# Performance work log

Hardware: AMD Instinct MI355X
Metric: run time of the kernel (lower is better)

The kernel has to match this reference:

```python
import jax, jax.numpy as jnp
import numpy as np
import math

D_MODEL = 1024
NUM_HEADS = 16
D_K = 64
B, T = 2, 2048


def setup_inputs() -> dict:
    key = jax.random.key(0)
    ks = jax.random.split(key, 12)
    s = 0.02
    return {
        "Q": jax.random.normal(ks[0], (B, T, D_MODEL), jnp.float32),
        "K": jax.random.normal(ks[1], (B, T, D_MODEL), jnp.float32),
        "V": jax.random.normal(ks[2], (B, T, D_MODEL), jnp.float32),
        # stacked per-head projection weights: [H, d_model, d_k]
        "Wq": jax.random.normal(ks[3], (NUM_HEADS, D_MODEL, D_K), jnp.float32) * s,
        "bq": jax.random.normal(ks[4], (NUM_HEADS, D_K), jnp.float32) * s,
        "Wk": jax.random.normal(ks[5], (NUM_HEADS, D_MODEL, D_K), jnp.float32) * s,
        "bk": jax.random.normal(ks[6], (NUM_HEADS, D_K), jnp.float32) * s,
        "Wv": jax.random.normal(ks[7], (NUM_HEADS, D_MODEL, D_K), jnp.float32) * s,
        "bv": jax.random.normal(ks[8], (NUM_HEADS, D_K), jnp.float32) * s,
        "Wo": jax.random.normal(ks[9], (D_MODEL, D_MODEL), jnp.float32) * s,
        "bo": jax.random.normal(ks[10], (D_MODEL,), jnp.float32) * s,
    }


def reference(Q, K, V, Wq, bq, Wk, bk, Wv, bv, Wo, bo):
    scale = 1.0 / math.sqrt(D_K)
    # fused batched per-head projections (replaces the Python per-head loop)
    Qh = jnp.einsum("btd,hdk->bhtk", Q, Wq) + bq[None, :, None, :]
    Kh = jnp.einsum("btd,hdk->bhtk", K, Wk) + bk[None, :, None, :]
    Vh = jnp.einsum("btd,hdk->bhtk", V, Wv) + bv[None, :, None, :]
    scores = jnp.einsum("bhtk,bhsk->bhts", Qh, Kh) * scale  # [B,H,T,T]
    attn = jax.nn.softmax(scores, axis=-1)
    ctx = jnp.einsum("bhts,bhsk->bhtk", attn, Vh)  # [B,H,T,d_k]
    # Faithful to the original: plain view of contiguous [B,H,T,d] into
    # [B,T,H*d] WITHOUT transposing head/time (matches torch .view semantics).
    bsz, nt = Q.shape[0], Q.shape[1]
    x = ctx.reshape(bsz, nt, NUM_HEADS * D_K)
    out = x @ Wo.T + bo
    # dropout with p=0.0 is identity; omitted for determinism
    return out
```

## Files before the change

kernel.cpp:

```cpp
#include <hip/hip_runtime.h>
#include <stdint.h>

typedef __attribute__((ext_vector_type(8))) short short8;
typedef __attribute__((ext_vector_type(4))) short short4v;
typedef __attribute__((ext_vector_type(4))) float float4v;

#define MFMA16(a, b, c) __builtin_amdgcn_mfma_f32_16x16x32_bf16((a), (b), (c), 0, 0, 0)

__device__ __forceinline__ ushort f2bf_rne(float f) {
  union { float f; unsigned u; } x; x.f = f;
  unsigned r = x.u + 0x7FFFu + ((x.u >> 16) & 1u);
  return (ushort)(r >> 16);
}
__device__ __forceinline__ ushort f2bf_trunc(float f) {
  union { float f; unsigned u; } x; x.f = f;
  return (ushort)(x.u >> 16);
}
__device__ __forceinline__ void gload16(const ushort* g, ushort* lds) {
  __builtin_amdgcn_global_load_lds(
      (__attribute__((address_space(1))) unsigned int*)g,
      (__attribute__((address_space(3))) unsigned int*)lds, 16, 0, 0);
}

__global__ __launch_bounds__(256) void cvt4_kernel(
    const float* __restrict__ s0, const float* __restrict__ s1,
    const float* __restrict__ s2, const float* __restrict__ s3,
    ushort* __restrict__ d0, ushort* __restrict__ d1, ushort* __restrict__ d2,
    ushort* __restrict__ d3) {
  const int plane = blockIdx.y;
  const int n = (plane == 3) ? (1 << 20) : (1 << 22);
  const int i = (blockIdx.x * 256 + threadIdx.x) * 8;
  if (i >= n) return;
  const float* s = plane == 0 ? s0 : (plane == 1 ? s1 : (plane == 2 ? s2 : s3));
  ushort* d = plane == 0 ? d0 : (plane == 1 ? d1 : (plane == 2 ? d2 : d3));
  float4 a = *(const float4*)(s + i);
  float4 b = *(const float4*)(s + i + 4);
  ushort t[8] __attribute__((aligned(16))) = {
      f2bf_rne(a.x), f2bf_rne(a.y), f2bf_rne(a.z), f2bf_rne(a.w),
      f2bf_rne(b.x), f2bf_rne(b.y), f2bf_rne(b.z), f2bf_rne(b.w)};
  *(uint4*)(d + i) = *(const uint4*)t;
}

__device__ __forceinline__ void transpose64f(const float* __restrict__ in, int is,
                                             ushort* __restrict__ out, int os,
                                             ushort* lds ) {
  const int t = threadIdx.x;
#pragma unroll
  for (int it = 0; it < 2; ++it) {
    int e = it * 2048 + t * 8;
    int r = e >> 6, c = e & 63;
    const float* p = in + (size_t)r * is + c;
    float4 x0 = *(const float4*)p;
    float4 x1 = *(const float4*)(p + 4);
    ushort tv[8] __attribute__((aligned(16))) = {
        f2bf_rne(x0.x), f2bf_rne(x0.y), f2bf_rne(x0.z), f2bf_rne(x0.w),
        f2bf_rne(x1.x), f2bf_rne(x1.y), f2bf_rne(x1.z), f2bf_rne(x1.w)};
    *(uint4*)&lds[r * 72 + c] = *(const uint4*)tv;
  }
  __syncthreads();
  const int cc = t >> 2;
  const int rg = (t & 3) * 16;
  ushort tmp[16] __attribute__((aligned(16)));
#pragma unroll
  for (int i = 0; i < 16; ++i) tmp[i] = lds[(rg + i) * 72 + cc];
  *(uint4*)&out[(size_t)cc * os + rg] = *(const uint4*)&tmp[0];
  *(uint4*)&out[(size_t)cc * os + rg + 8] = *(const uint4*)&tmp[8];
}

__global__ __launch_bounds__(256, 2) void repack_w_kernel(
    const float* __restrict__ Wq, const float* __restrict__ Wk,
    const float* __restrict__ Wv, ushort* __restrict__ BtQ, ushort* __restrict__ BtK,
    ushort* __restrict__ BtV) {
  __shared__ ushort lds[64 * 72];
  const float* W = blockIdx.z == 0 ? Wq : (blockIdx.z == 1 ? Wk : Wv);
  ushort* Bt = blockIdx.z == 0 ? BtQ : (blockIdx.z == 1 ? BtK : BtV);
  const int h = blockIdx.y, dt = blockIdx.x;
  transpose64f(W + h * 65536 + dt * 4096, 64, Bt + h * 65536 + dt * 64, 1024, lds);
}

template <int F32>
__device__ __forceinline__ void stage16(const void* G, size_t eoff, ushort* ldst) {
  if (F32) {
    const float* p = (const float*)G + eoff;
    float4 x0 = *(const float4*)p;
    float4 x1 = *(const float4*)(p + 4);
    ushort t[8] __attribute__((aligned(16))) = {
        f2bf_rne(x0.x), f2bf_rne(x0.y), f2bf_rne(x0.z), f2bf_rne(x0.w),
        f2bf_rne(x1.x), f2bf_rne(x1.y), f2bf_rne(x1.z), f2bf_rne(x1.w)};
    *(uint4*)ldst = *(const uint4*)t;
  } else {
    gload16((const ushort*)G + eoff, ldst);
  }
}

template <int AF32, int BF32>
__device__ __forceinline__ void gemm_body(const void* __restrict__ A,
                                          const void* __restrict__ Bt,
                                          const float* __restrict__ bias,
                                          void* __restrict__ C, int cmode, float ascale,
                                          int N, int K, ushort* lA, ushort* lB) {
  const int tid = threadIdx.x;
  const int l = tid & 63, lane15 = l & 15, quad = l >> 4;
  const int mbase = blockIdx.y * 128, nbase = blockIdx.x * 128;
  const int w = tid >> 6;
  const int wrow = (w >> 1) * 64, wcol = (w & 1) * 64;

  const int e0 = tid * 8;
  const int e1 = 2048 + tid * 8;
  const int r0 = e0 >> 5, c0 = e0 & 31;
  const int r1 = e1 >> 5, c1 = e1 & 31;

  float4v acc[4][4];
#pragma unroll
  for (int i = 0; i < 4; ++i)
#pragma unroll
    for (int j = 0; j < 4; ++j) acc[i][j] = (float4v){0.f, 0.f, 0.f, 0.f};

  for (int kb = 0; kb < K; kb += 32) {
    __syncthreads();
    stage16<AF32>(A, (size_t)(mbase + r0) * K + c0 + kb, &lA[e0]);
    stage16<AF32>(A, (size_t)(mbase + r1) * K + c1 + kb, &lA[e1]);
    stage16<BF32>(Bt, (size_t)(nbase + r0) * K + c0 + kb, &lB[e0]);
    stage16<BF32>(Bt, (size_t)(nbase + r1) * K + c1 + kb, &lB[e1]);
    asm volatile("s_waitcnt vmcnt(0)" ::: "memory");
    __syncthreads();
    short8 a[4], b[4];
#pragma unroll
    for (int i = 0; i < 4; ++i) {
      a[i] = *(const short8*)&lA[(wrow + i * 16 + lane15) * 32 + quad * 8];
      b[i] = *(const short8*)&lB[(wcol + i * 16 + lane15) * 32 + quad * 8];
    }
#pragma unroll
    for (int i = 0; i < 4; ++i)
#pragma unroll
      for (int j = 0; j < 4; ++j) acc[i][j] = MFMA16(a[i], b[j], acc[i][j]);
  }

#pragma unroll
  for (int j = 0; j < 4; ++j) {
    const int n = nbase + wcol + j * 16 + lane15;
    const float bvs = bias[n];
#pragma unroll
    for (int i = 0; i < 4; ++i) {
      const int m0 = mbase + wrow + i * 16 + quad * 4;
#pragma unroll
      for (int r = 0; r < 4; ++r) {
        const float val = (acc[i][j][r] + bvs) * ascale;
        if (cmode == 1) {
          const int m = m0 + r;
          const int bb = m >> 11, t = m & 2047;
          const int hh = n >> 6, dk = n & 63;
          ((ushort*)C)[((size_t)(((bb << 4) + hh) * 64 + dk)) * 2048 + t] = f2bf_rne(val);
        } else if (cmode == 2) {
          ((float*)C)[(size_t)(m0 + r) * N + n] = val;
        } else {
          ((ushort*)C)[(size_t)(m0 + r) * N + n] = f2bf_rne(val);
        }
      }
    }
  }
}

#define CEXP 0.1803368801111204f

__global__ __launch_bounds__(256, 2) void proj3_kernel(
    const ushort* __restrict__ Qb, const ushort* __restrict__ Kb,
    const ushort* __restrict__ Vb, const ushort* __restrict__ BtQ,
    const ushort* __restrict__ BtK, const ushort* __restrict__ BtV,
    const float* __restrict__ bq, const float* __restrict__ bk,
    const float* __restrict__ bv, ushort* __restrict__ Qh, ushort* __restrict__ Kh,
    ushort* __restrict__ Vt) {
  __shared__ ushort lA[128 * 32], lB[128 * 32];
  if (blockIdx.z == 0)
    gemm_body<0, 0>(Qb, BtQ, bq, Qh, 0, CEXP, 1024, 1024, lA, lB);
  else if (blockIdx.z == 1)
    gemm_body<0, 0>(Kb, BtK, bk, Kh, 0, 1.0f, 1024, 1024, lA, lB);
  else
    gemm_body<0, 0>(Vb, BtV, bv, Vt, 1, 1.0f, 1024, 1024, lA, lB);
}

__global__ __launch_bounds__(256, 2) void proj3f_kernel(
    const float* __restrict__ Q, const float* __restrict__ Kin,
    const float* __restrict__ V, const ushort* __restrict__ BtQ,
    const ushort* __restrict__ BtK, const ushort* __restrict__ BtV,
    const float* __restrict__ bq, const float* __restrict__ bk,
    const float* __restrict__ bv, ushort* __restrict__ Qh, ushort* __restrict__ Kh,
    ushort* __restrict__ Vt) {
  __shared__ ushort lA[128 * 32], lB[128 * 32];
  if (blockIdx.z == 0)
    gemm_body<1, 0>(Q, BtQ, bq, Qh, 0, CEXP, 1024, 1024, lA, lB);
  else if (blockIdx.z == 1)
    gemm_body<1, 0>(Kin, BtK, bk, Kh, 0, 1.0f, 1024, 1024, lA, lB);
  else
    gemm_body<1, 0>(V, BtV, bv, Vt, 1, 1.0f, 1024, 1024, lA, lB);
}

__global__ __launch_bounds__(256, 2) void gemm_bt_kernel(
    const ushort* __restrict__ X, const ushort* __restrict__ WoB,
    const float* __restrict__ bo, float* __restrict__ out) {
  __shared__ ushort lA[128 * 32], lB[128 * 32];
  gemm_body<0, 0>(X, WoB, bo, out, 2, 1.0f, 1024, 1024, lA, lB);
}

__global__ __launch_bounds__(256, 2) void gemm_btf_kernel(
    const ushort* __restrict__ X, const float* __restrict__ Wo,
    const float* __restrict__ bo, float* __restrict__ out) {
  __shared__ ushort lA[128 * 32], lB[128 * 32];
  gemm_body<0, 1>(X, Wo, bo, out, 2, 1.0f, 1024, 1024, lA, lB);
}

__global__ __launch_bounds__(256, 4) void attn_kernel(const ushort* __restrict__ Qh,
                                                      const ushort* __restrict__ Kh,
                                                      const ushort* __restrict__ Vt,
                                                      ushort* __restrict__ ctxout) {
  __shared__ ushort lK[64 * 64];
  __shared__ ushort lV[64 * 64];
  __shared__ ushort pl_all[4][16 * 68];
  const int tid = threadIdx.x, l = tid & 63, wv = tid >> 6;
  const int lane15 = l & 15, quad = l >> 4;
  const int bh = blockIdx.x, b = bh >> 4, h = bh & 15;
  const int q0 = blockIdx.y * 64 + wv * 16;

  const int sr = tid >> 3;
  const int scb = (tid & 7) ^ (sr & 7);
  const ushort* Kp = Kh + (size_t)(b * 2048) * 1024 + h * 64;
  const ushort* Vp = Vt + (size_t)(bh * 64) * 2048;
  const ushort* Kg0 = Kp + (size_t)sr * 1024 + scb * 8;
  const ushort* Kg1 = Kg0 + 32 * 1024;
  const ushort* Vg0 = Vp + (size_t)sr * 2048 + scb * 8;
  const ushort* Vg1 = Vg0 + 32 * 2048;
  ushort* lKd0 = lK + tid * 8;
  ushort* lKd1 = lK + 2048 + tid * 8;
  ushort* lVd0 = lV + tid * 8;
  ushort* lVd1 = lV + 2048 + tid * 8;

  const ushort* qrow = Qh + (size_t)(b * 2048 + q0 + lane15) * 1024 + h * 64;
  const short8 qa0 = *(const short8*)&qrow[quad * 8];
  const short8 qa1 = *(const short8*)&qrow[32 + quad * 8];

  const int xm = lane15 & 7;
  const int fr0 = lane15 * 64 + ((quad ^ xm) * 8);
  const int fr1 = lane15 * 64 + (((quad + 4) ^ xm) * 8);

  ushort* pl = &pl_all[wv][0];
  const short8 ones = {0x3F80, 0x3F80, 0x3F80, 0x3F80, 0x3F80, 0x3F80, 0x3F80, 0x3F80};

  float4v o[4];
  float4v lf = (float4v){0.f, 0.f, 0.f, 0.f};
#pragma unroll
  for (int i = 0; i < 4; ++i) o[i] = (float4v){0.f, 0.f, 0.f, 0.f};

  for (int s0 = 0; s0 < 2048; s0 += 64) {
    __syncthreads();
    gload16(Kg0 + (size_t)s0 * 1024, lKd0);
    gload16(Kg1 + (size_t)s0 * 1024, lKd1);
    gload16(Vg0 + s0, lVd0);
    gload16(Vg1 + s0, lVd1);
    asm volatile("s_waitcnt vmcnt(0)" ::: "memory");
    __syncthreads();

    float4v sb[4];
#pragma unroll
    for (int i = 0; i < 4; ++i) {
      short8 k0 = *(const short8*)&lK[i * 1024 + fr0];
      short8 k1 = *(const short8*)&lK[i * 1024 + fr1];
      float4v c = (float4v){0.f, 0.f, 0.f, 0.f};
      c = MFMA16(qa0, k0, c);
      c = MFMA16(qa1, k1, c);
      sb[i] = c;
    }
#pragma unroll
    for (int i = 0; i < 4; ++i)
#pragma unroll
      for (int r = 0; r < 4; ++r)
        pl[(quad * 4 + r) * 68 + i * 16 + lane15] =
            f2bf_trunc(__builtin_amdgcn_exp2f(sb[i][r]));
    short4v p0a = *(const short4v*)&pl[lane15 * 68 + quad * 8];
    short4v p0b = *(const short4v*)&pl[lane15 * 68 + quad * 8 + 4];
    short4v p1a = *(const short4v*)&pl[lane15 * 68 + 32 + quad * 8];
    short4v p1b = *(const short4v*)&pl[lane15 * 68 + 32 + quad * 8 + 4];
    short8 pa0 = __builtin_shufflevector(p0a, p0b, 0, 1, 2, 3, 4, 5, 6, 7);
    short8 pa1 = __builtin_shufflevector(p1a, p1b, 0, 1, 2, 3, 4, 5, 6, 7);
    lf = MFMA16(pa0, ones, lf);
    lf = MFMA16(pa1, ones, lf);
#pragma unroll
    for (int nf = 0; nf < 4; ++nf) {
      short8 v0 = *(const short8*)&lV[nf * 1024 + fr0];
      short8 v1 = *(const short8*)&lV[nf * 1024 + fr1];
      o[nf] = MFMA16(pa0, v0, o[nf]);
      o[nf] = MFMA16(pa1, v1, o[nf]);
    }
  }

  float inv[4];
#pragma unroll
  for (int r = 0; r < 4; ++r) inv[r] = (lf[r] > 0.f) ? 1.0f / lf[r] : 0.0f;
  ushort* crow = ctxout + ((size_t)bh * 2048 + q0) * 64;
#pragma unroll
  for (int nf = 0; nf < 4; ++nf)
#pragma unroll
    for (int r = 0; r < 4; ++r)
      crow[(size_t)(quad * 4 + r) * 64 + nf * 16 + lane15] = f2bf_rne(o[nf][r] * inv[r]);
}

extern "C" void kernel_launch(void* const* d_in, const int* in_sizes, int n_in,
                              void* d_out, int out_size, void* d_ws, size_t ws_size,
                              hipStream_t stream) {
  const float* Q = (const float*)d_in[0];
  const float* K = (const float*)d_in[1];
  const float* V = (const float*)d_in[2];
  const float* Wq = (const float*)d_in[3];
  const float* bq = (const float*)d_in[4];
  const float* Wk = (const float*)d_in[5];
  const float* bk = (const float*)d_in[6];
  const float* Wv = (const float*)d_in[7];
  const float* bv = (const float*)d_in[8];
  const float* Wo = (const float*)d_in[9];
  const float* bo = (const float*)d_in[10];
  float* out = (float*)d_out;
  ushort* ws = (ushort*)d_ws;

  if (ws_size >= (58ull << 20)) {
    ushort* Qh = ws;
    ushort* Kh = Qh + (4 << 20);
    ushort* Vt = Kh + (4 << 20);
    ushort* BtQ = Vt + (4 << 20);
    ushort* BtK = BtQ + (1 << 20);
    ushort* BtV = BtK + (1 << 20);
    ushort* X = BtQ;
    ushort* WoB = ws + (16ull << 20);
    ushort* Qb = WoB + (1 << 20);
    ushort* Kb = Qb + (4 << 20);
    ushort* Vb = Kb + (4 << 20);

    cvt4_kernel<<<dim3(2048, 4), 256, 0, stream>>>(Q, K, V, Wo, Qb, Kb, Vb, WoB);
    repack_w_kernel<<<dim3(16, 16, 3), 256, 0, stream>>>(Wq, Wk, Wv, BtQ, BtK, BtV);
    proj3_kernel<<<dim3(8, 32, 3), 256, 0, stream>>>(Qb, Kb, Vb, BtQ, BtK, BtV, bq, bk,
                                                     bv, Qh, Kh, Vt);
    attn_kernel<<<dim3(32, 32), 256, 0, stream>>>(Qh, Kh, Vt, X);
    gemm_bt_kernel<<<dim3(8, 32), 256, 0, stream>>>(X, WoB, bo, out);
  } else {
    ushort* Qh = ws;
    ushort* Kh = Qh + (4 << 20);
    ushort* Vt = Kh + (4 << 20);
    ushort* R = Vt + (4 << 20);
    ushort* BtQ = R;
    ushort* BtK = R + (1 << 20);
    ushort* BtV = R + (2 << 20);
    ushort* X = R;

    repack_w_kernel<<<dim3(16, 16, 3), 256, 0, stream>>>(Wq, Wk, Wv, BtQ, BtK, BtV);
    proj3f_kernel<<<dim3(8, 32, 3), 256, 0, stream>>>(Q, K, V, BtQ, BtK, BtV, bq, bk, bv,
                                                      Qh, Kh, Vt);
    attn_kernel<<<dim3(32, 32), 256, 0, stream>>>(Qh, Kh, Vt, X);
    gemm_btf_kernel<<<dim3(8, 32), 256, 0, stream>>>(X, Wo, bo, out);
  }
}
```

Before: 239.5 us.

## Double-buffer LDS in GEMM and attention, merge prep kernels, coalesce V-transpose stores

Merges the input-conversion and weight-repack launches into one prep kernel. Adds a double-buffered LDS GEMM path that prefetches the next K-tile with async global-to-LDS loads while the MFMAs run on the current tile, and uses it for the projection and output GEMMs. The transposed V output is staged through LDS so it can be written with 16-byte stores. Attention also double-buffers its K/V tiles and drops its occupancy hint from 4 to 3 to fit the larger LDS footprint. That lowers occupancy and relies on hand-written waitcnt/barrier ordering.

```diff
diff --git a/kernel.cpp b/kernel.cpp
--- a/kernel.cpp
+++ b/kernel.cpp
@@ -22,24 +22,7 @@
       (__attribute__((address_space(3))) unsigned int*)lds, 16, 0, 0);
 }
 
-__global__ __launch_bounds__(256) void cvt4_kernel(
-    const float* __restrict__ s0, const float* __restrict__ s1,
-    const float* __restrict__ s2, const float* __restrict__ s3,
-    ushort* __restrict__ d0, ushort* __restrict__ d1, ushort* __restrict__ d2,
-    ushort* __restrict__ d3) {
-  const int plane = blockIdx.y;
-  const int n = (plane == 3) ? (1 << 20) : (1 << 22);
-  const int i = (blockIdx.x * 256 + threadIdx.x) * 8;
-  if (i >= n) return;
-  const float* s = plane == 0 ? s0 : (plane == 1 ? s1 : (plane == 2 ? s2 : s3));
-  ushort* d = plane == 0 ? d0 : (plane == 1 ? d1 : (plane == 2 ? d2 : d3));
-  float4 a = *(const float4*)(s + i);
-  float4 b = *(const float4*)(s + i + 4);
-  ushort t[8] __attribute__((aligned(16))) = {
-      f2bf_rne(a.x), f2bf_rne(a.y), f2bf_rne(a.z), f2bf_rne(a.w),
-      f2bf_rne(b.x), f2bf_rne(b.y), f2bf_rne(b.z), f2bf_rne(b.w)};
-  *(uint4*)(d + i) = *(const uint4*)t;
-}
+#define CEXP 0.1803368801111204f
 
 __device__ __forceinline__ void transpose64f(const float* __restrict__ in, int is,
                                              ushort* __restrict__ out, int os,
@@ -67,6 +50,44 @@
   *(uint4*)&out[(size_t)cc * os + rg + 8] = *(const uint4*)&tmp[8];
 }
 
+__global__ __launch_bounds__(256) void prep_kernel(
+    const float* __restrict__ Q, const float* __restrict__ K,
+    const float* __restrict__ V, const float* __restrict__ Wo,
+    const float* __restrict__ Wq, const float* __restrict__ Wk,
+    const float* __restrict__ Wv, ushort* __restrict__ Qb, ushort* __restrict__ Kb,
+    ushort* __restrict__ Vb, ushort* __restrict__ WoB, ushort* __restrict__ BtQ,
+    ushort* __restrict__ BtK, ushort* __restrict__ BtV) {
+  __shared__ ushort lds[64 * 72];
+  const int bx = blockIdx.x;
+  if (bx < 6656) {
+    const float* s;
+    ushort* d;
+    int i;
+    if (bx < 6144) {
+      const int plane = bx >> 11;
+      s = plane == 0 ? Q : (plane == 1 ? K : V);
+      d = plane == 0 ? Qb : (plane == 1 ? Kb : Vb);
+      i = ((bx & 2047) * 256 + threadIdx.x) * 8;
+    } else {
+      s = Wo;
+      d = WoB;
+      i = ((bx - 6144) * 256 + threadIdx.x) * 8;
+    }
+    float4 a = *(const float4*)(s + i);
+    float4 b = *(const float4*)(s + i + 4);
+    ushort t[8] __attribute__((aligned(16))) = {
+        f2bf_rne(a.x), f2bf_rne(a.y), f2bf_rne(a.z), f2bf_rne(a.w),
+        f2bf_rne(b.x), f2bf_rne(b.y), f2bf_rne(b.z), f2bf_rne(b.w)};
+    *(uint4*)(d + i) = *(const uint4*)t;
+  } else {
+    const int rb = bx - 6656;
+    const int dt = rb & 15, h = (rb >> 4) & 15, z = rb >> 8;
+    const float* W = z == 0 ? Wq : (z == 1 ? Wk : Wv);
+    ushort* Bt = z == 0 ? BtQ : (z == 1 ? BtK : BtV);
+    transpose64f(W + h * 65536 + dt * 4096, 64, Bt + h * 65536 + dt * 64, 1024, lds);
+  }
+}
+
 __global__ __launch_bounds__(256, 2) void repack_w_kernel(
     const float* __restrict__ Wq, const float* __restrict__ Wk,
     const float* __restrict__ Wv, ushort* __restrict__ BtQ, ushort* __restrict__ BtK,
@@ -76,6 +97,137 @@
   ushort* Bt = blockIdx.z == 0 ? BtQ : (blockIdx.z == 1 ? BtK : BtV);
   const int h = blockIdx.y, dt = blockIdx.x;
   transpose64f(W + h * 65536 + dt * 4096, 64, Bt + h * 65536 + dt * 64, 1024, lds);
+}
+
+__device__ __forceinline__ void gemm_pipe(const ushort* __restrict__ A,
+                                          const ushort* __restrict__ Bt,
+                                          const float* __restrict__ bias,
+                                          void* __restrict__ C, int cmode, float ascale,
+                                          int N, int K, ushort* lA, ushort* lB) {
+  const int tid = threadIdx.x;
+  const int l = tid & 63, lane15 = l & 15, quad = l >> 4;
+  const int mbase = blockIdx.y * 128, nbase = blockIdx.x * 128;
+  const int wv = tid >> 6;
+  const int wrow = (wv >> 1) * 64, wcol = (wv & 1) * 64;
+
+  const int e0 = tid * 8;
+  const int e1 = 2048 + tid * 8;
+  const int r0 = e0 >> 5, c0 = e0 & 31;
+  const int r1 = e1 >> 5, c1 = e1 & 31;
+  const ushort* Ag0 = A + (size_t)(mbase + r0) * K + c0;
+  const ushort* Ag1 = A + (size_t)(mbase + r1) * K + c1;
+  const ushort* Bg0 = Bt + (size_t)(nbase + r0) * K + c0;
+  const ushort* Bg1 = Bt + (size_t)(nbase + r1) * K + c1;
+
+  float4v acc[4][4];
+#pragma unroll
+  for (int i = 0; i < 4; ++i)
+#pragma unroll
+    for (int j = 0; j < 4; ++j) acc[i][j] = (float4v){0.f, 0.f, 0.f, 0.f};
+
+  gload16(Ag0, lA + e0);
+  gload16(Ag1, lA + e1);
+  gload16(Bg0, lB + e0);
+  gload16(Bg1, lB + e1);
+
+  for (int kb = 0; kb < K; kb += 32) {
+    const int p = (kb >> 5) & 1;
+    const int kn = (kb + 32 < K) ? kb + 32 : 0;
+    const int q = (p ^ 1) * 4096;
+    gload16(Ag0 + kn, lA + q + e0);
+    gload16(Ag1 + kn, lA + q + e1);
+    gload16(Bg0 + kn, lB + q + e0);
+    gload16(Bg1 + kn, lB + q + e1);
+    asm volatile("s_waitcnt vmcnt(4)\ns_barrier" ::: "memory");
+    const int base = p * 4096;
+    short8 a[4], b[4];
+#pragma unroll
+    for (int i = 0; i < 4; ++i) {
+      a[i] = *(const short8*)&lA[base + (wrow + i * 16 + lane15) * 32 + quad * 8];
+      b[i] = *(const short8*)&lB[base + (wcol + i * 16 + lane15) * 32 + quad * 8];
+    }
+#pragma unroll
+    for (int i = 0; i < 4; ++i)
+#pragma unroll
+      for (int j = 0; j < 4; ++j) acc[i][j] = MFMA16(a[i], b[j], acc[i][j]);
+    asm volatile("s_waitcnt lgkmcnt(0)\ns_barrier" ::: "memory");
+  }
+
+  if (cmode == 1) {
+    asm volatile("s_waitcnt vmcnt(0) lgkmcnt(0)\ns_barrier" ::: "memory");
+    uint* sp = (uint*)lA + wv * 576;
+    const int bb = mbase >> 11;
+    const int tb = (mbase & 2047) + wrow;
+#pragma unroll
+    for (int j = 0; j < 4; ++j) {
+      {
+        const int n = nbase + wcol + j * 16 + lane15;
+        const float bvs = bias[n];
+#pragma unroll
+        for (int i = 0; i < 4; ++i)
+#pragma unroll
+          for (int rp = 0; rp < 2; ++rp) {
+            const uint lo = f2bf_rne((acc[i][j][2 * rp] + bvs) * ascale);
+            const uint hi = f2bf_rne((acc[i][j][2 * rp + 1] + bvs) * ascale);
+            sp[36 * lane15 + i * 8 + quad * 2 + rp] = lo | (hi << 16);
+          }
+      }
+#pragma unroll
+      for (int t = 0; t < 2; ++t) {
+        const int row = t * 8 + (l >> 3);
+        const int c = l & 7;
+        uint4 d = *(const uint4*)(sp + 36 * row + 4 * c);
+        const int ng = nbase + wcol + j * 16 + row;
+        ushort* dst = (ushort*)C + ((size_t)(bb * 1024 + ng)) * 2048 + tb + c * 8;
+        *(uint4*)dst = d;
+      }
+    }
+    return;
+  }
+
+#pragma unroll
+  for (int j = 0; j < 4; ++j) {
+    const int n = nbase + wcol + j * 16 + lane15;
+    const float bvs = bias[n];
+#pragma unroll
+    for (int i = 0; i < 4; ++i) {
+      const int m0 = mbase + wrow + i * 16 + quad * 4;
+#pragma unroll
+      for (int r = 0; r < 4; ++r) {
+        const float val = (acc[i][j][r] + bvs) * ascale;
+        if (cmode == 2)
+          ((float*)C)[(size_t)(m0 + r) * N + n] = val;
+        else
+          ((ushort*)C)[(size_t)(m0 + r) * N + n] = f2bf_rne(val);
+      }
+    }
+  }
+}
+
+__global__ __launch_bounds__(256, 2) void proj3_kernel(
+    const ushort* __restrict__ Qb, const ushort* __restrict__ Kb,
+    const ushort* __restrict__ Vb, const ushort* __restrict__ BtQ,
+    const ushort* __restrict__ BtK, const ushort* __restrict__ BtV,
+    const float* __restrict__ bq, const float* __restrict__ bk,
+    const float* __restrict__ bv, ushort* __restrict__ Qh, ushort* __restrict__ Kh,
+    ushort* __restrict__ Vt) {
+  __shared__ ushort lA[2 * 4096], lB[2 * 4096];
+  const ushort *Aop, *Bop;
+  const float* bs;
+  ushort* Cp;
+  int cm;
+  float as;
+  if (blockIdx.z == 0) { Aop = Qb; Bop = BtQ; bs = bq; Cp = Qh; cm = 0; as = CEXP; }
+  else if (blockIdx.z == 1) { Aop = Kb; Bop = BtK; bs = bk; Cp = Kh; cm = 0; as = 1.0f; }
+  else { Aop = Vb; Bop = BtV; bs = bv; Cp = Vt; cm = 1; as = 1.0f; }
+  gemm_pipe(Aop, Bop, bs, Cp, cm, as, 1024, 1024, lA, lB);
+}
+
+__global__ __launch_bounds__(256, 2) void gemm_bt_kernel(
+    const ushort* __restrict__ X, const ushort* __restrict__ WoB,
+    const float* __restrict__ bo, float* __restrict__ out) {
+  __shared__ ushort lA[2 * 4096], lB[2 * 4096];
+  gemm_pipe(X, WoB, bo, out, 2, 1.0f, 1024, 1024, lA, lB);
 }
 
 template <int F32>
@@ -94,17 +246,17 @@
 }
 
 template <int AF32, int BF32>
-__device__ __forceinline__ void gemm_body(const void* __restrict__ A,
-                                          const void* __restrict__ Bt,
-                                          const float* __restrict__ bias,
-                                          void* __restrict__ C, int cmode, float ascale,
-                                          int N, int K, ushort* lA, ushort* lB) {
+__device__ __forceinline__ void gemm_body_basic(const void* __restrict__ A,
+                                                const void* __restrict__ Bt,
+                                                const float* __restrict__ bias,
+                                                void* __restrict__ C, int cmode,
+                                                float ascale, int N, int K, ushort* lA,
+                                                ushort* lB) {
   const int tid = threadIdx.x;
   const int l = tid & 63, lane15 = l & 15, quad = l >> 4;
   const int mbase = blockIdx.y * 128, nbase = blockIdx.x * 128;
   const int w = tid >> 6;
   const int wrow = (w >> 1) * 64, wcol = (w & 1) * 64;
-
   const int e0 = tid * 8;
   const int e1 = 2048 + tid * 8;
   const int r0 = e0 >> 5, c0 = e0 & 31;
@@ -149,8 +301,7 @@
         if (cmode == 1) {
           const int m = m0 + r;
           const int bb = m >> 11, t = m & 2047;
-          const int hh = n >> 6, dk = n & 63;
-          ((ushort*)C)[((size_t)(((bb << 4) + hh) * 64 + dk)) * 2048 + t] = f2bf_rne(val);
+          ((ushort*)C)[((size_t)(bb * 1024 + n)) * 2048 + t] = f2bf_rne(val);
         } else if (cmode == 2) {
           ((float*)C)[(size_t)(m0 + r) * N + n] = val;
         } else {
@@ -159,24 +310,6 @@
       }
     }
   }
-}
-
-#define CEXP 0.1803368801111204f
-
-__global__ __launch_bounds__(256, 2) void proj3_kernel(
-    const ushort* __restrict__ Qb, const ushort* __restrict__ Kb,
-    const ushort* __restrict__ Vb, const ushort* __restrict__ BtQ,
-    const ushort* __restrict__ BtK, const ushort* __restrict__ BtV,
-    const float* __restrict__ bq, const float* __restrict__ bk,
-    const float* __restrict__ bv, ushort* __restrict__ Qh, ushort* __restrict__ Kh,
-    ushort* __restrict__ Vt) {
-  __shared__ ushort lA[128 * 32], lB[128 * 32];
-  if (blockIdx.z == 0)
-    gemm_body<0, 0>(Qb, BtQ, bq, Qh, 0, CEXP, 1024, 1024, lA, lB);
-  else if (blockIdx.z == 1)
-    gemm_body<0, 0>(Kb, BtK, bk, Kh, 0, 1.0f, 1024, 1024, lA, lB);
-  else
-    gemm_body<0, 0>(Vb, BtV, bv, Vt, 1, 1.0f, 1024, 1024, lA, lB);
 }
 
 __global__ __launch_bounds__(256, 2) void proj3f_kernel(
@@ -188,33 +321,26 @@
     ushort* __restrict__ Vt) {
   __shared__ ushort lA[128 * 32], lB[128 * 32];
   if (blockIdx.z == 0)
-    gemm_body<1, 0>(Q, BtQ, bq, Qh, 0, CEXP, 1024, 1024, lA, lB);
+    gemm_body_basic<1, 0>(Q, BtQ, bq, Qh, 0, CEXP, 1024, 1024, lA, lB);
   else if (blockIdx.z == 1)
-    gemm_body<1, 0>(Kin, BtK, bk, Kh, 0, 1.0f, 1024, 1024, lA, lB);
+    gemm_body_basic<1, 0>(Kin, BtK, bk, Kh, 0, 1.0f, 1024, 1024, lA, lB);
   else
-    gemm_body<1, 0>(V, BtV, bv, Vt, 1, 1.0f, 1024, 1024, lA, lB);
-}
-
-__global__ __launch_bounds__(256, 2) void gemm_bt_kernel(
-    const ushort* __restrict__ X, const ushort* __restrict__ WoB,
-    const float* __restrict__ bo, float* __restrict__ out) {
-  __shared__ ushort lA[128 * 32], lB[128 * 32];
-  gemm_body<0, 0>(X, WoB, bo, out, 2, 1.0f, 1024, 1024, lA, lB);
+    gemm_body_basic<1, 0>(V, BtV, bv, Vt, 1, 1.0f, 1024, 1024, lA, lB);
 }
 
 __global__ __launch_bounds__(256, 2) void gemm_btf_kernel(
     const ushort* __restrict__ X, const float* __restrict__ Wo,
     const float* __restrict__ bo, float* __restrict__ out) {
   __shared__ ushort lA[128 * 32], lB[128 * 32];
-  gemm_body<0, 1>(X, Wo, bo, out, 2, 1.0f, 1024, 1024, lA, lB);
-}
-
-__global__ __launch_bounds__(256, 4) void attn_kernel(const ushort* __restrict__ Qh,
+  gemm_body_basic<0, 1>(X, Wo, bo, out, 2, 1.0f, 1024, 1024, lA, lB);
+}
+
+__global__ __launch_bounds__(256, 3) void attn_kernel(const ushort* __restrict__ Qh,
                                                       const ushort* __restrict__ Kh,
                                                       const ushort* __restrict__ Vt,
                                                       ushort* __restrict__ ctxout) {
-  __shared__ ushort lK[64 * 64];
-  __shared__ ushort lV[64 * 64];
+  __shared__ ushort lK[2 * 4096];
+  __shared__ ushort lV[2 * 4096];
   __shared__ ushort pl_all[4][16 * 68];
   const int tid = threadIdx.x, l = tid & 63, wv = tid >> 6;
   const int lane15 = l & 15, quad = l >> 4;
@@ -229,10 +355,6 @@
   const ushort* Kg1 = Kg0 + 32 * 1024;
   const ushort* Vg0 = Vp + (size_t)sr * 2048 + scb * 8;
   const ushort* Vg1 = Vg0 + 32 * 2048;
-  ushort* lKd0 = lK + tid * 8;
-  ushort* lKd1 = lK + 2048 + tid * 8;
-  ushort* lVd0 = lV + tid * 8;
-  ushort* lVd1 = lV + 2048 + tid * 8;
 
   const ushort* qrow = Qh + (size_t)(b * 2048 + q0 + lane15) * 1024 + h * 64;
   const short8 qa0 = *(const short8*)&qrow[quad * 8];
@@ -250,20 +372,27 @@
 #pragma unroll
   for (int i = 0; i < 4; ++i) o[i] = (float4v){0.f, 0.f, 0.f, 0.f};
 
+  gload16(Kg0, lK + tid * 8);
+  gload16(Kg1, lK + 2048 + tid * 8);
+  gload16(Vg0, lV + tid * 8);
+  gload16(Vg1, lV + 2048 + tid * 8);
+
   for (int s0 = 0; s0 < 2048; s0 += 64) {
-    __syncthreads();
-    gload16(Kg0 + (size_t)s0 * 1024, lKd0);
-    gload16(Kg1 + (size_t)s0 * 1024, lKd1);
-    gload16(Vg0 + s0, lVd0);
-    gload16(Vg1 + s0, lVd1);
-    asm volatile("s_waitcnt vmcnt(0)" ::: "memory");
-    __syncthreads();
+    const int p = (s0 >> 6) & 1;
+    const int sn = (s0 + 64 < 2048) ? s0 + 64 : 0;
+    const int q = (p ^ 1) * 4096;
+    gload16(Kg0 + (size_t)sn * 1024, lK + q + tid * 8);
+    gload16(Kg1 + (size_t)sn * 1024, lK + q + 2048 + tid * 8);
+    gload16(Vg0 + sn, lV + q + tid * 8);
+    gload16(Vg1 + sn, lV + q + 2048 + tid * 8);
+    asm volatile("s_waitcnt vmcnt(4)\ns_barrier" ::: "memory");
+    const int base = p * 4096;
 
     float4v sb[4];
 #pragma unroll
     for (int i = 0; i < 4; ++i) {
-      short8 k0 = *(const short8*)&lK[i * 1024 + fr0];
-      short8 k1 = *(const short8*)&lK[i * 1024 + fr1];
+      short8 k0 = *(const short8*)&lK[base + i * 1024 + fr0];
+      short8 k1 = *(const short8*)&lK[base + i * 1024 + fr1];
       float4v c = (float4v){0.f, 0.f, 0.f, 0.f};
       c = MFMA16(qa0, k0, c);
       c = MFMA16(qa1, k1, c);
@@ -285,11 +414,12 @@
     lf = MFMA16(pa1, ones, lf);
 #pragma unroll
     for (int nf = 0; nf < 4; ++nf) {
-      short8 v0 = *(const short8*)&lV[nf * 1024 + fr0];
-      short8 v1 = *(const short8*)&lV[nf * 1024 + fr1];
+      short8 v0 = *(const short8*)&lV[base + nf * 1024 + fr0];
+      short8 v1 = *(const short8*)&lV[base + nf * 1024 + fr1];
       o[nf] = MFMA16(pa0, v0, o[nf]);
       o[nf] = MFMA16(pa1, v1, o[nf]);
     }
+    asm volatile("s_waitcnt lgkmcnt(0)\ns_barrier" ::: "memory");
   }
 
   float inv[4];
@@ -333,8 +463,8 @@
     ushort* Kb = Qb + (4 << 20);
     ushort* Vb = Kb + (4 << 20);
 
-    cvt4_kernel<<<dim3(2048, 4), 256, 0, stream>>>(Q, K, V, Wo, Qb, Kb, Vb, WoB);
-    repack_w_kernel<<<dim3(16, 16, 3), 256, 0, stream>>>(Wq, Wk, Wv, BtQ, BtK, BtV);
+    prep_kernel<<<dim3(7424), 256, 0, stream>>>(Q, K, V, Wo, Wq, Wk, Wv, Qb, Kb, Vb,
+                                                WoB, BtQ, BtK, BtV);
     proj3_kernel<<<dim3(8, 32, 3), 256, 0, stream>>>(Qb, Kb, Vb, BtQ, BtK, BtV, bq, bk,
                                                      bv, Qh, Kh, Vt);
     attn_kernel<<<dim3(32, 32), 256, 0, stream>>>(Qh, Kh, Vt, X);
```

New measurement: 243.6 us. Within noise of the previous version (+1.7%).
